# Performance work log

Hardware: AMD Instinct MI355X
Metric: run time of the kernel (lower is better)

## Reference

```python
import jax, jax.numpy as jnp
import numpy as np

B, S, D, H = 4, 2048, 512, 8
HD = D // H

def setup_inputs() -> dict:
    key = jax.random.key(0)
    ks = jax.random.split(key, 11)
    sc = 0.02
    inp = {
        'query': jax.random.normal(ks[0], (B, S, D), jnp.float32),
        'key':   jax.random.normal(ks[1], (B, S, D), jnp.float32),
        'value': jax.random.normal(ks[2], (B, S, D), jnp.float32),
        # causal boolean mask, broadcastable to (B, H, S, S)
        'mask':  jnp.tril(jnp.ones((S, S), bool))[None, None],
        'wq': jax.random.normal(ks[3], (D, D), jnp.float32) * sc,
        'bq': jnp.zeros((D,), jnp.float32),
        'wk': jax.random.normal(ks[4], (D, D), jnp.float32) * sc,
        'bk': jnp.zeros((D,), jnp.float32),
        'wv': jax.random.normal(ks[5], (D, D), jnp.float32) * sc,
        'bv': jnp.zeros((D,), jnp.float32),
        'wo': jax.random.normal(ks[6], (D, D), jnp.float32) * sc,
        'bo': jnp.zeros((D,), jnp.float32),
    }
    return inp


def reference(query, key, value, mask, wq, bq, wk, bk, wv, bv, wo, bo):
    b, s, d = query.shape

    def proj(x, w, bias):
        # torch nn.Linear: x @ W^T + b, then split heads -> (B, H, L, HD)
        y = x @ w.T + bias
        return y.reshape(b, -1, H, HD).transpose(0, 2, 1, 3)

    q = proj(query, wq, bq)   # (B,H,S,HD)
    k = proj(key,   wk, bk)
    v = proj(value, wv, bv)

    scores = jnp.einsum('bhqd,bhkd->bhqk', q, k) / np.sqrt(HD).astype(jnp.float32)
    scores = jnp.where(mask, scores, -jnp.inf)
    # torch code subtracts rowmax then softmaxes; jax.nn.softmax is the same stable form
    attn = jax.nn.softmax(scores, axis=-1)  # dropout p=0.0 -> identity
    out = jnp.einsum('bhqk,bhkd->bhqd', attn, v)
    out = out.transpose(0, 2, 1, 3).reshape(b, s, d)
    return out @ wo.T + bo
```

## Files before the change

### kernel.cpp

```cpp
#include <hip/hip_runtime.h>

#define NB 4
#define NS 2048
#define ND 512
#define NH 8
#define NHD 64
#define NM (NB*NS)

using bf16 = __bf16;
using bf16x8 = __bf16 __attribute__((ext_vector_type(8)));
using f32x4 = float __attribute__((ext_vector_type(4)));

static_assert(sizeof(bf16x8) == 16, "bf16x8 must be 16B");

typedef __attribute__((address_space(1))) void glob_t;
typedef __attribute__((address_space(3))) void lds_t;

__device__ __forceinline__ void stage16_f32(const float* __restrict__ src, bf16* dst) {
    float4 f0 = *(const float4*)(src + 0);
    float4 f1 = *(const float4*)(src + 4);
    float4 f2 = *(const float4*)(src + 8);
    float4 f3 = *(const float4*)(src + 12);
    bf16x8 v0, v1;
    v0[0]=(bf16)f0.x; v0[1]=(bf16)f0.y; v0[2]=(bf16)f0.z; v0[3]=(bf16)f0.w;
    v0[4]=(bf16)f1.x; v0[5]=(bf16)f1.y; v0[6]=(bf16)f1.z; v0[7]=(bf16)f1.w;
    v1[0]=(bf16)f2.x; v1[1]=(bf16)f2.y; v1[2]=(bf16)f2.z; v1[3]=(bf16)f2.w;
    v1[4]=(bf16)f3.x; v1[5]=(bf16)f3.y; v1[6]=(bf16)f3.z; v1[7]=(bf16)f3.w;
    *(bf16x8*)dst       = v0;
    *(bf16x8*)(dst + 8) = v1;
}

template<bool A_BF16, bool HEAD_OUT>
__device__ __forceinline__ void gemm_body(bf16* As, bf16* Bs, const void* __restrict__ Ap,
        const float* __restrict__ W, const float* __restrict__ bias, void* __restrict__ outp)
{
    constexpr int LP = 40;
    const int tid  = threadIdx.x;
    const int lane = tid & 63;
    const int wid  = tid >> 6;
    const int wm = wid >> 1, wn = wid & 1;
    const int lr = lane & 15, lg = lane >> 4;
    const int m0 = blockIdx.x * 128, n0 = blockIdx.y * 128;

    const int srow = tid >> 1;
    const int scol = (tid & 1) << 4;

    f32x4 acc[4][4] = {};

    for (int k0 = 0; k0 < ND; k0 += 32) {
        if (A_BF16) {
            const bf16* src = (const bf16*)Ap + (size_t)(m0 + srow) * ND + k0 + scol;
            *(uint4*)&As[srow * LP + scol]     = *(const uint4*)(src);
            *(uint4*)&As[srow * LP + scol + 8] = *(const uint4*)(src + 8);
        } else {
            const float* src = (const float*)Ap + (size_t)(m0 + srow) * ND + k0 + scol;
            stage16_f32(src, &As[srow * LP + scol]);
        }
        {
            const float* src = W + (size_t)(n0 + srow) * ND + k0 + scol;
            stage16_f32(src, &Bs[srow * LP + scol]);
        }
        __syncthreads();

        bf16x8 af[4], bfr[4];
        #pragma unroll
        for (int i = 0; i < 4; i++)
            af[i] = *(const bf16x8*)&As[(wm * 64 + i * 16 + lr) * LP + lg * 8];
        #pragma unroll
        for (int i = 0; i < 4; i++)
            bfr[i] = *(const bf16x8*)&Bs[(wn * 64 + i * 16 + lr) * LP + lg * 8];

        #pragma unroll
        for (int mf = 0; mf < 4; mf++)
            #pragma unroll
            for (int nf = 0; nf < 4; nf++)
                acc[mf][nf] = __builtin_amdgcn_mfma_f32_16x16x32_bf16(
                        af[mf], bfr[nf], acc[mf][nf], 0, 0, 0);
        __syncthreads();
    }

    float bv[4];
    #pragma unroll
    for (int nf = 0; nf < 4; nf++)
        bv[nf] = bias[n0 + wn * 64 + nf * 16 + lr];

    #pragma unroll
    for (int mf = 0; mf < 4; mf++) {
        #pragma unroll
        for (int nf = 0; nf < 4; nf++) {
            const int col = n0 + wn * 64 + nf * 16 + lr;
            #pragma unroll
            for (int r = 0; r < 4; r++) {
                const int row = m0 + wm * 64 + mf * 16 + lg * 4 + r;
                const float v = acc[mf][nf][r] + bv[nf];
                if (HEAD_OUT) {
                    const int b  = row >> 11;
                    const int s  = row & (NS - 1);
                    const int hh = col >> 6;
                    const int hd = col & (NHD - 1);
                    ((bf16*)outp)[(((size_t)b * NH + hh) * NS + s) * NHD + hd] = (bf16)v;
                } else {
                    ((float*)outp)[(size_t)row * ND + col] = v;
                }
            }
        }
    }
}

__global__ __launch_bounds__(256) void gemm_proj3(
        const float* __restrict__ q, const float* __restrict__ k, const float* __restrict__ v,
        const float* __restrict__ wq, const float* __restrict__ wk, const float* __restrict__ wv,
        const float* __restrict__ bq, const float* __restrict__ bk, const float* __restrict__ bv,
        bf16* __restrict__ qb, bf16* __restrict__ kb, bf16* __restrict__ vb)
{
    __shared__ __align__(16) bf16 As[128 * 40];
    __shared__ __align__(16) bf16 Bs[128 * 40];
    const int z = blockIdx.z;
    const float* A = (z == 0) ? q  : (z == 1) ? k  : v;
    const float* W = (z == 0) ? wq : (z == 1) ? wk : wv;
    const float* B = (z == 0) ? bq : (z == 1) ? bk : bv;
    bf16*        o = (z == 0) ? qb : (z == 1) ? kb : vb;
    gemm_body<false, true>(As, Bs, A, W, B, o);
}

__global__ __launch_bounds__(256) void gemm_out(const bf16* __restrict__ A,
        const float* __restrict__ W, const float* __restrict__ b, float* __restrict__ out)
{
    __shared__ __align__(16) bf16 As[128 * 40];
    __shared__ __align__(16) bf16 Bs[128 * 40];
    gemm_body<true, false>(As, Bs, A, W, b, out);
}

#define QSCALE 0.18033688011112042f

__device__ __forceinline__ void stage_k(const bf16* __restrict__ src_base,
                                        bf16* dst_base, int w, int lane) {
    #pragma unroll
    for (int j = 0; j < 2; j++) {
        const int c   = (w * 2 + j) * 64 + lane;
        const int row = c >> 3;
        const int cs  = (c & 7) ^ (row & 7);
        const bf16* src = src_base + row * NHD + cs * 8;
        __builtin_amdgcn_global_load_lds((const glob_t*)src,
                (lds_t*)(dst_base + (w * 2 + j) * 512), 16, 0, 0);
    }
}

__device__ __forceinline__ void stage_v_write(bf16* dst, int c8, int r2,
                                              bf16x8 v0, bf16x8 v1) {
    const unsigned short* a0 = (const unsigned short*)&v0;
    const unsigned short* a1 = (const unsigned short*)&v1;
    #pragma unroll
    for (int j = 0; j < 8; j++) {
        const int hd = c8 * 8 + j;
        int byte = hd * 128 + r2 * 2;
        byte ^= (hd & 7) << 4;
        *(unsigned int*)((char*)dst + byte) = (unsigned int)a0[j] | ((unsigned int)a1[j] << 16);
    }
}

__global__ __launch_bounds__(256) void attn_kern(const bf16* __restrict__ Qg,
        const bf16* __restrict__ Kg, const bf16* __restrict__ Vg,
        bf16* __restrict__ Og)
{
    __shared__ __align__(16) bf16 Kt[2][64 * 64];
    __shared__ __align__(16) bf16 Vt[2][64 * 64];
    __shared__ __align__(16) bf16 Pl[4][32 * 64];

    const int b = blockIdx.z, h = blockIdx.y;
    const int q0 = (gridDim.x - 1 - blockIdx.x) * 128;
    const int tid = threadIdx.x;
    const int lane = tid & 63, w = tid >> 6;
    const int lr = lane & 15, lg = lane >> 4;

    const size_t bh = ((size_t)b * NH + h) * NS;
    const bf16* Kb = Kg + bh * NHD;
    const bf16* Vb = Vg + bh * NHD;

    const int c8 = tid >> 5;
    const int r2 = (tid & 31) * 2;

    bf16x8 qf[2][2];
    #pragma unroll
    for (int rf = 0; rf < 2; rf++) {
        const bf16* qp = Qg + (bh + q0 + w * 32 + rf * 16 + lr) * NHD;
        #pragma unroll
        for (int kk = 0; kk < 2; kk++) {
            bf16x8 t = *(const bf16x8*)(qp + kk * 32 + lg * 8);
            #pragma unroll
            for (int j = 0; j < 8; j++)
                qf[rf][kk][j] = (bf16)((float)t[j] * QSCALE);
        }
    }

    f32x4 acc_o[2][4] = {};
    float l_lane[2][4] = {};

    const int ntiles = q0 / 64 + 2;
    const int wrow0 = q0 + w * 32;
    const int wrow_max = wrow0 + 31;

    stage_k(Kb, &Kt[0][0], w, lane);
    {
        bf16x8 v0 = *(const bf16x8*)(Vb + (size_t)r2 * NHD + c8 * 8);
        bf16x8 v1 = *(const bf16x8*)(Vb + (size_t)(r2 + 1) * NHD + c8 * 8);
        stage_v_write(&Vt[0][0], c8, r2, v0, v1);
    }
    __syncthreads();

    int cur = 0;
    for (int t = 0; t < ntiles; t++) {
        const int kv0 = t * 64;
        const bool have_next = (t + 1 < ntiles);
        bf16x8 nv0, nv1;
        if (have_next) {
            const int nkv = kv0 + 64;
            stage_k(Kb + (size_t)nkv * NHD, &Kt[cur ^ 1][0], w, lane);
            nv0 = *(const bf16x8*)(Vb + (size_t)(nkv + r2) * NHD + c8 * 8);
            nv1 = *(const bf16x8*)(Vb + (size_t)(nkv + r2 + 1) * NHD + c8 * 8);
        }

        if (kv0 <= wrow_max) {
            f32x4 s[2][4];
            #pragma unroll
            for (int rf = 0; rf < 2; rf++)
                #pragma unroll
                for (int nf = 0; nf < 4; nf++) {
                    f32x4 a = {};
                    #pragma unroll
                    for (int kk = 0; kk < 2; kk++) {
                        const int row = nf * 16 + lr;
                        int byte = row * 128 + (kk * 32 + lg * 8) * 2;
                        byte ^= (row & 7) << 4;
                        bf16x8 kf = *(const bf16x8*)((const char*)&Kt[cur][0] + byte);
                        a = __builtin_amdgcn_mfma_f32_16x16x32_bf16(qf[rf][kk], kf, a, 0, 0, 0);
                    }
                    s[rf][nf] = a;
                }

            if (kv0 + 63 > wrow0) {
                #pragma unroll
                for (int rf = 0; rf < 2; rf++)
                    #pragma unroll
                    for (int nf = 0; nf < 4; nf++) {
                        const int col = kv0 + nf * 16 + lr;
                        #pragma unroll
                        for (int rr = 0; rr < 4; rr++) {
                            const int row = wrow0 + rf * 16 + lg * 4 + rr;
                            if (col > row) s[rf][nf][rr] = -1e30f;
                        }
                    }
            }

            #pragma unroll
            for (int rf = 0; rf < 2; rf++)
                #pragma unroll
                for (int nf = 0; nf < 4; nf++)
                    #pragma unroll
                    for (int rr = 0; rr < 4; rr++) {
                        const float p = __builtin_amdgcn_exp2f(s[rf][nf][rr]);
                        l_lane[rf][rr] += p;
                        const int prow = rf * 16 + lg * 4 + rr;
                        int byte = prow * 128 + (nf * 16 + lr) * 2;
                        byte ^= (prow & 7) << 4;
                        *(bf16*)((char*)&Pl[w][0] + byte) = (bf16)p;
                    }

            bf16x8 pf[2][2];
            #pragma unroll
            for (int rf = 0; rf < 2; rf++)
                #pragma unroll
                for (int kk = 0; kk < 2; kk++) {
                    const int row = rf * 16 + lr;
                    int byte = row * 128 + (kk * 32 + lg * 8) * 2;
                    byte ^= (row & 7) << 4;
                    pf[rf][kk] = *(const bf16x8*)((char*)&Pl[w][0] + byte);
                }
            #pragma unroll
            for (int hf = 0; hf < 4; hf++) {
                #pragma unroll
                for (int kk = 0; kk < 2; kk++) {
                    const int row = hf * 16 + lr;
                    int byte = row * 128 + (kk * 32 + lg * 8) * 2;
                    byte ^= (row & 7) << 4;
                    bf16x8 vf = *(const bf16x8*)((const char*)&Vt[cur][0] + byte);
                    acc_o[0][hf] = __builtin_amdgcn_mfma_f32_16x16x32_bf16(pf[0][kk], vf, acc_o[0][hf], 0, 0, 0);
                    acc_o[1][hf] = __builtin_amdgcn_mfma_f32_16x16x32_bf16(pf[1][kk], vf, acc_o[1][hf], 0, 0, 0);
                }
            }
        }

        if (have_next)
            stage_v_write(&Vt[cur ^ 1][0], c8, r2, nv0, nv1);
        __syncthreads();
        cur ^= 1;
    }

    #pragma unroll
    for (int rf = 0; rf < 2; rf++)
        #pragma unroll
        for (int rr = 0; rr < 4; rr++) {
            float l = l_lane[rf][rr];
            l += __shfl_xor(l, 1);
            l += __shfl_xor(l, 2);
            l += __shfl_xor(l, 4);
            l += __shfl_xor(l, 8);
            l_lane[rf][rr] = 1.0f / l;
        }

    #pragma unroll
    for (int rf = 0; rf < 2; rf++)
        #pragma unroll
        for (int hf = 0; hf < 4; hf++) {
            const int col = h * NHD + hf * 16 + lr;
            #pragma unroll
            for (int rr = 0; rr < 4; rr++) {
                const int srow = wrow0 + rf * 16 + lg * 4 + rr;
                Og[((size_t)b * NS + srow) * ND + col] =
                        (bf16)(acc_o[rf][hf][rr] * l_lane[rf][rr]);
            }
        }
}

extern "C" void kernel_launch(void* const* d_in, const int* in_sizes, int n_in,
                              void* d_out, int out_size, void* d_ws, size_t ws_size,
                              hipStream_t stream) {
    const float* query = (const float*)d_in[0];
    const float* key   = (const float*)d_in[1];
    const float* value = (const float*)d_in[2];
    const float* wq = (const float*)d_in[4];
    const float* bq = (const float*)d_in[5];
    const float* wk = (const float*)d_in[6];
    const float* bk = (const float*)d_in[7];
    const float* wv = (const float*)d_in[8];
    const float* bv = (const float*)d_in[9];
    const float* wo = (const float*)d_in[10];
    const float* bo = (const float*)d_in[11];
    float* out = (float*)d_out;

    bf16* qb = (bf16*)d_ws;
    bf16* kb = qb + (size_t)NM * ND;
    bf16* vb = kb + (size_t)NM * ND;
    bf16* ob = vb + (size_t)NM * ND;

    gemm_proj3<<<dim3(NM / 128, ND / 128, 3), 256, 0, stream>>>(
            query, key, value, wq, wk, wv, bq, bk, bv, qb, kb, vb);

    attn_kern<<<dim3(NS / 128, NH, NB), 256, 0, stream>>>(qb, kb, vb, ob);

    gemm_out<<<dim3(NM / 128, ND / 128), 256, 0, stream>>>(ob, wo, bo, out);
}
```

Before: 128.6 us.

## Keep attention probabilities in registers via transposed S and 16x16x16 MFMA

The attention kernel now computes S transposed (K as the A operand), so the exp'd probabilities land directly in the register layout that a 16x16x16 bf16 MFMA expects for the PV product. This removes the per-warp LDS round-trip for P. Blocks shrink to 64 query rows with 128 threads and are scheduled in an interleaved heavy/light order to balance the causal workload. Staging and V transpose are reorganized, and MFMA priority is raised around the PV loop. The trade-offs are twice as many blocks that each reload K/V tiles, and more MFMA instructions of a smaller shape.

```diff
diff --git a/kernel.cpp b/kernel.cpp
--- a/kernel.cpp
+++ b/kernel.cpp
@@ -10,11 +10,17 @@
 using bf16 = __bf16;
 using bf16x8 = __bf16 __attribute__((ext_vector_type(8)));
 using f32x4 = float __attribute__((ext_vector_type(4)));
+using i16x4 = short __attribute__((ext_vector_type(4)));
 
 static_assert(sizeof(bf16x8) == 16, "bf16x8 must be 16B");
+static_assert(sizeof(i16x4) == 8, "i16x4 must be 8B");
 
 typedef __attribute__((address_space(1))) void glob_t;
 typedef __attribute__((address_space(3))) void lds_t;
+
+__device__ __forceinline__ void mfma16(f32x4& c, i16x4 a, i16x4 b) {
+    asm("v_mfma_f32_16x16x16_bf16 %0, %1, %2, %0" : "+v"(c) : "v"(a), "v"(b));
+}
 
 __device__ __forceinline__ void stage16_f32(const float* __restrict__ src, bf16* dst) {
     float4 f0 = *(const float4*)(src + 0);
@@ -133,42 +139,16 @@
 
 #define QSCALE 0.18033688011112042f
 
-__device__ __forceinline__ void stage_k(const bf16* __restrict__ src_base,
-                                        bf16* dst_base, int w, int lane) {
-    #pragma unroll
-    for (int j = 0; j < 2; j++) {
-        const int c   = (w * 2 + j) * 64 + lane;
-        const int row = c >> 3;
-        const int cs  = (c & 7) ^ (row & 7);
-        const bf16* src = src_base + row * NHD + cs * 8;
-        __builtin_amdgcn_global_load_lds((const glob_t*)src,
-                (lds_t*)(dst_base + (w * 2 + j) * 512), 16, 0, 0);
-    }
-}
-
-__device__ __forceinline__ void stage_v_write(bf16* dst, int c8, int r2,
-                                              bf16x8 v0, bf16x8 v1) {
-    const unsigned short* a0 = (const unsigned short*)&v0;
-    const unsigned short* a1 = (const unsigned short*)&v1;
-    #pragma unroll
-    for (int j = 0; j < 8; j++) {
-        const int hd = c8 * 8 + j;
-        int byte = hd * 128 + r2 * 2;
-        byte ^= (hd & 7) << 4;
-        *(unsigned int*)((char*)dst + byte) = (unsigned int)a0[j] | ((unsigned int)a1[j] << 16);
-    }
-}
-
-__global__ __launch_bounds__(256) void attn_kern(const bf16* __restrict__ Qg,
+__global__ __launch_bounds__(128) void attn_kern(const bf16* __restrict__ Qg,
         const bf16* __restrict__ Kg, const bf16* __restrict__ Vg,
         bf16* __restrict__ Og)
 {
     __shared__ __align__(16) bf16 Kt[2][64 * 64];
     __shared__ __align__(16) bf16 Vt[2][64 * 64];
-    __shared__ __align__(16) bf16 Pl[4][32 * 64];
 
     const int b = blockIdx.z, h = blockIdx.y;
-    const int q0 = (gridDim.x - 1 - blockIdx.x) * 128;
+    const int x = blockIdx.x;
+    const int qb = (x & 1) ? ((x - 1) >> 1) : (31 - (x >> 1));
     const int tid = threadIdx.x;
     const int lane = tid & 63, w = tid >> 6;
     const int lr = lane & 15, lg = lane >> 4;
@@ -177,13 +157,22 @@
     const bf16* Kb = Kg + bh * NHD;
     const bf16* Vb = Vg + bh * NHD;
 
-    const int c8 = tid >> 5;
-    const int r2 = (tid & 31) * 2;
+    int ksrc[4];
+    #pragma unroll
+    for (int j = 0; j < 4; j++) {
+        const int c   = (w * 4 + j) * 64 + lane;
+        const int row = c >> 3;
+        const int cs  = (c & 7) ^ (row & 7);
+        ksrc[j] = row * NHD + cs * 8;
+    }
+
+    const int c8 = tid >> 4;
+    const int r0 = (tid & 15) * 4;
 
     bf16x8 qf[2][2];
     #pragma unroll
     for (int rf = 0; rf < 2; rf++) {
-        const bf16* qp = Qg + (bh + q0 + w * 32 + rf * 16 + lr) * NHD;
+        const bf16* qp = Qg + (bh + qb * 64 + w * 32 + rf * 16 + lr) * NHD;
         #pragma unroll
         for (int kk = 0; kk < 2; kk++) {
             bf16x8 t = *(const bf16x8*)(qp + kk * 32 + lg * 8);
@@ -194,132 +183,138 @@
     }
 
     f32x4 acc_o[2][4] = {};
-    float l_lane[2][4] = {};
-
-    const int ntiles = q0 / 64 + 2;
-    const int wrow0 = q0 + w * 32;
-    const int wrow_max = wrow0 + 31;
-
-    stage_k(Kb, &Kt[0][0], w, lane);
-    {
-        bf16x8 v0 = *(const bf16x8*)(Vb + (size_t)r2 * NHD + c8 * 8);
-        bf16x8 v1 = *(const bf16x8*)(Vb + (size_t)(r2 + 1) * NHD + c8 * 8);
-        stage_v_write(&Vt[0][0], c8, r2, v0, v1);
-    }
+    float l_lane[2] = {0.f, 0.f};
+
+    const int qrow0 = qb * 64 + w * 32;
+    const int ntiles = qb + 1;
+
+    auto stage = [&](int buf, int kv0) {
+        #pragma unroll
+        for (int j = 0; j < 4; j++)
+            __builtin_amdgcn_global_load_lds(
+                (const glob_t*)(Kb + (size_t)kv0 * NHD + ksrc[j]),
+                (lds_t*)(&Kt[buf][(w * 4 + j) * 512]), 16, 0, 0);
+        bf16x8 vv[4];
+        #pragma unroll
+        for (int i = 0; i < 4; i++)
+            vv[i] = *(const bf16x8*)(Vb + (size_t)(kv0 + r0 + i) * NHD + c8 * 8);
+        #pragma unroll
+        for (int j = 0; j < 8; j++) {
+            const int hd = c8 * 8 + j;
+            int byte = hd * 128 + r0 * 2;
+            byte ^= (hd & 7) << 4;
+            i16x4 pk;
+            #pragma unroll
+            for (int i = 0; i < 4; i++) {
+                bf16 hval = vv[i][j];
+                pk[i] = (short)__builtin_bit_cast(unsigned short, hval);
+            }
+            *(i16x4*)((char*)&Vt[buf][0] + byte) = pk;
+        }
+    };
+
+    stage(0, 0);
     __syncthreads();
 
     int cur = 0;
     for (int t = 0; t < ntiles; t++) {
         const int kv0 = t * 64;
-        const bool have_next = (t + 1 < ntiles);
-        bf16x8 nv0, nv1;
-        if (have_next) {
-            const int nkv = kv0 + 64;
-            stage_k(Kb + (size_t)nkv * NHD, &Kt[cur ^ 1][0], w, lane);
-            nv0 = *(const bf16x8*)(Vb + (size_t)(nkv + r2) * NHD + c8 * 8);
-            nv1 = *(const bf16x8*)(Vb + (size_t)(nkv + r2 + 1) * NHD + c8 * 8);
-        }
-
-        if (kv0 <= wrow_max) {
-            f32x4 s[2][4];
-            #pragma unroll
-            for (int rf = 0; rf < 2; rf++)
+        if (t + 1 < ntiles) stage(cur ^ 1, kv0 + 64);
+
+        f32x4 s[4][2];
+        #pragma unroll
+        for (int nf = 0; nf < 4; nf++) {
+            bf16x8 kf[2];
+            #pragma unroll
+            for (int kk = 0; kk < 2; kk++) {
+                const int row = nf * 16 + lr;
+                int byte = row * 128 + (kk * 32 + lg * 8) * 2;
+                byte ^= (row & 7) << 4;
+                kf[kk] = *(const bf16x8*)((const char*)&Kt[cur][0] + byte);
+            }
+            #pragma unroll
+            for (int rf = 0; rf < 2; rf++) {
+                f32x4 a = {};
+                a = __builtin_amdgcn_mfma_f32_16x16x32_bf16(kf[0], qf[rf][0], a, 0, 0, 0);
+                a = __builtin_amdgcn_mfma_f32_16x16x32_bf16(kf[1], qf[rf][1], a, 0, 0, 0);
+                s[nf][rf] = a;
+            }
+        }
+
+        i16x4 pa[2][4];
+        if (kv0 + 63 > qrow0) {
+            #pragma unroll
+            for (int rf = 0; rf < 2; rf++) {
+                const int qg = qrow0 + rf * 16 + lr;
                 #pragma unroll
-                for (int nf = 0; nf < 4; nf++) {
-                    f32x4 a = {};
+                for (int nf = 0; nf < 4; nf++)
                     #pragma unroll
-                    for (int kk = 0; kk < 2; kk++) {
-                        const int row = nf * 16 + lr;
-                        int byte = row * 128 + (kk * 32 + lg * 8) * 2;
-                        byte ^= (row & 7) << 4;
-                        bf16x8 kf = *(const bf16x8*)((const char*)&Kt[cur][0] + byte);
-                        a = __builtin_amdgcn_mfma_f32_16x16x32_bf16(qf[rf][kk], kf, a, 0, 0, 0);
+                    for (int rr = 0; rr < 4; rr++) {
+                        const int kvg = kv0 + nf * 16 + lg * 4 + rr;
+                        float sv = s[nf][rf][rr];
+                        sv = (kvg > qg) ? -1e30f : sv;
+                        const float p = __builtin_amdgcn_exp2f(sv);
+                        l_lane[rf] += p;
+                        bf16 ph = (bf16)p;
+                        pa[rf][nf][rr] = (short)__builtin_bit_cast(unsigned short, ph);
                     }
-                    s[rf][nf] = a;
-                }
-
-            if (kv0 + 63 > wrow0) {
-                #pragma unroll
-                for (int rf = 0; rf < 2; rf++)
-                    #pragma unroll
-                    for (int nf = 0; nf < 4; nf++) {
-                        const int col = kv0 + nf * 16 + lr;
-                        #pragma unroll
-                        for (int rr = 0; rr < 4; rr++) {
-                            const int row = wrow0 + rf * 16 + lg * 4 + rr;
-                            if (col > row) s[rf][nf][rr] = -1e30f;
-                        }
-                    }
-            }
-
+            }
+        } else {
             #pragma unroll
             for (int rf = 0; rf < 2; rf++)
                 #pragma unroll
                 for (int nf = 0; nf < 4; nf++)
                     #pragma unroll
                     for (int rr = 0; rr < 4; rr++) {
-                        const float p = __builtin_amdgcn_exp2f(s[rf][nf][rr]);
-                        l_lane[rf][rr] += p;
-                        const int prow = rf * 16 + lg * 4 + rr;
-                        int byte = prow * 128 + (nf * 16 + lr) * 2;
-                        byte ^= (prow & 7) << 4;
-                        *(bf16*)((char*)&Pl[w][0] + byte) = (bf16)p;
+                        const float p = __builtin_amdgcn_exp2f(s[nf][rf][rr]);
+                        l_lane[rf] += p;
+                        bf16 ph = (bf16)p;
+                        pa[rf][nf][rr] = (short)__builtin_bit_cast(unsigned short, ph);
                     }
-
-            bf16x8 pf[2][2];
-            #pragma unroll
-            for (int rf = 0; rf < 2; rf++)
+        }
+
+        i16x4 vf[4][4];
+        #pragma unroll
+        for (int hf = 0; hf < 4; hf++)
+            #pragma unroll
+            for (int nf = 0; nf < 4; nf++) {
+                const int hd = hf * 16 + lr;
+                int byte = hd * 128 + (nf * 16 + lg * 4) * 2;
+                byte ^= (hd & 7) << 4;
+                vf[hf][nf] = *(const i16x4*)((const char*)&Vt[cur][0] + byte);
+            }
+
+        __builtin_amdgcn_s_setprio(1);
+        #pragma unroll
+        for (int rf = 0; rf < 2; rf++)
+            #pragma unroll
+            for (int hf = 0; hf < 4; hf++)
                 #pragma unroll
-                for (int kk = 0; kk < 2; kk++) {
-                    const int row = rf * 16 + lr;
-                    int byte = row * 128 + (kk * 32 + lg * 8) * 2;
-                    byte ^= (row & 7) << 4;
-                    pf[rf][kk] = *(const bf16x8*)((char*)&Pl[w][0] + byte);
-                }
-            #pragma unroll
-            for (int hf = 0; hf < 4; hf++) {
-                #pragma unroll
-                for (int kk = 0; kk < 2; kk++) {
-                    const int row = hf * 16 + lr;
-                    int byte = row * 128 + (kk * 32 + lg * 8) * 2;
-                    byte ^= (row & 7) << 4;
-                    bf16x8 vf = *(const bf16x8*)((const char*)&Vt[cur][0] + byte);
-                    acc_o[0][hf] = __builtin_amdgcn_mfma_f32_16x16x32_bf16(pf[0][kk], vf, acc_o[0][hf], 0, 0, 0);
-                    acc_o[1][hf] = __builtin_amdgcn_mfma_f32_16x16x32_bf16(pf[1][kk], vf, acc_o[1][hf], 0, 0, 0);
-                }
-            }
-        }
-
-        if (have_next)
-            stage_v_write(&Vt[cur ^ 1][0], c8, r2, nv0, nv1);
+                for (int nf = 0; nf < 4; nf++)
+                    mfma16(acc_o[rf][hf], pa[rf][nf], vf[hf][nf]);
+        __builtin_amdgcn_s_setprio(0);
+
         __syncthreads();
         cur ^= 1;
     }
 
     #pragma unroll
-    for (int rf = 0; rf < 2; rf++)
+    for (int rf = 0; rf < 2; rf++) {
+        float l = l_lane[rf];
+        l += __shfl_xor(l, 16);
+        l += __shfl_xor(l, 32);
+        const float linv = 1.0f / l;
         #pragma unroll
         for (int rr = 0; rr < 4; rr++) {
-            float l = l_lane[rf][rr];
-            l += __shfl_xor(l, 1);
-            l += __shfl_xor(l, 2);
-            l += __shfl_xor(l, 4);
-            l += __shfl_xor(l, 8);
-            l_lane[rf][rr] = 1.0f / l;
-        }
-
-    #pragma unroll
-    for (int rf = 0; rf < 2; rf++)
-        #pragma unroll
-        for (int hf = 0; hf < 4; hf++) {
-            const int col = h * NHD + hf * 16 + lr;
-            #pragma unroll
-            for (int rr = 0; rr < 4; rr++) {
-                const int srow = wrow0 + rf * 16 + lg * 4 + rr;
-                Og[((size_t)b * NS + srow) * ND + col] =
-                        (bf16)(acc_o[rf][hf][rr] * l_lane[rf][rr]);
-            }
-        }
+            const float li = __shfl(linv, lg * 4 + rr, 16);
+            const int row = qrow0 + rf * 16 + lg * 4 + rr;
+            #pragma unroll
+            for (int hf = 0; hf < 4; hf++) {
+                const int col = h * NHD + hf * 16 + lr;
+                Og[((size_t)b * NS + row) * ND + col] = (bf16)(acc_o[rf][hf][rr] * li);
+            }
+        }
+    }
 }
 
 extern "C" void kernel_launch(void* const* d_in, const int* in_sizes, int n_in,
@@ -346,7 +341,7 @@
     gemm_proj3<<<dim3(NM / 128, ND / 128, 3), 256, 0, stream>>>(
             query, key, value, wq, wk, wv, bq, bk, bv, qb, kb, vb);
 
-    attn_kern<<<dim3(NS / 128, NH, NB), 256, 0, stream>>>(qb, kb, vb, ob);
+    attn_kern<<<dim3(NS / 64, NH, NB), 128, 0, stream>>>(qb, kb, vb, ob);
 
     gemm_out<<<dim3(NM / 128, ND / 128), 256, 0, stream>>>(ob, wo, bo, out);
 }
```

After: 127.1 us (median of 2 runs). No clear change (-1.2%).
